# Performance work log

Measured on AMD Instinct MI355X. Metric: run time of the kernel, lower is better.

## Reference

```python
import jax, jax.numpy as jnp
import numpy as np
import itertools

N_SUBSETS = 4
TAU = 0.1


def setup_inputs() -> dict:
    key = jax.random.key(0)
    k1, k2, k3 = jax.random.split(key, 3)
    # scale projections so exp(sim/tau) stays numerically sane (module assumes small/normalized projections)
    projections = jax.random.normal(k1, (8192, 128), dtype=jnp.float32) * 0.05
    xrecon = jax.random.normal(k2, (8192, 784), dtype=jnp.float32)
    recon_label = jax.random.normal(k3, (8192, 784), dtype=jnp.float32)
    return {"projections": projections, "xrecon": xrecon, "recon_label": recon_label}


def _joint_loss(projections, xrecon, recon_label):
    # reconstruction MSE
    recon_loss = jnp.mean(jnp.square(xrecon - recon_label))

    # ---- XNegloss (SimCLR-style with n_subsets positives per group) ----
    N, D = projections.shape
    sim = (projections @ projections.T) / TAU  # [N, N] dot similarity
    gid = jnp.arange(N) // N_SUBSETS
    pos_mask = gid[:, None] == gid[None, :]  # same-group entries are positives
    exp_sim = jnp.exp(sim)
    # original code drops positive entries exactly equal to 1 (positives[positives != 1])
    pos_sum = jnp.sum(jnp.where(pos_mask & (sim != 1.0), exp_sim, 0.0), axis=-1)
    neg_sum = jnp.sum(jnp.where(pos_mask, 0.0, exp_sim), axis=-1)
    closs = jnp.mean(-jnp.log(pos_sum / (pos_sum + neg_sum)))

    # ---- distance loss: MSE over all subset pairs within each group ----
    combi = np.array(list(itertools.combinations(range(N_SUBSETS), 2)))
    left, right = combi[:, 0], combi[:, 1]
    P = projections.reshape(N // N_SUBSETS, N_SUBSETS, D)
    # per-group mean over (pairs, D) then mean over groups == global mean (equal counts)
    dist_loss = jnp.mean(jnp.square(P[:, left] - P[:, right]))

    loss = recon_loss + closs + dist_loss
    return loss, closs, recon_loss, dist_loss


def reference(projections, xrecon, recon_label):
    return _joint_loss(projections, xrecon, recon_label)
```

## Files before the change

kernel.cpp:

```cpp
#include <hip/hip_runtime.h>
#include <hip/hip_bf16.h>
#include <stdint.h>

typedef __bf16 bf16x8 __attribute__((ext_vector_type(8)));
typedef float  f32x4  __attribute__((ext_vector_type(4)));

#define NROWS   8192
#define DIMK    128
#define NGROUPS 2048
#define RECON_N 6422528
#define SIM_BLOCKS   1024
#define RECON_BLOCKS 1568
#define GROUP_BLOCKS 512
#define FUSED_BLOCKS 3104

#define WS_SP     0
#define WS_G      131072
#define WS_E      139264
#define WS_RPART  147456
#define WS_DPART  149024
#define WS_PB     149536

__device__ __forceinline__ void async16(const void* g, void* l) {
    __builtin_amdgcn_global_load_lds(
        (const __attribute__((address_space(1))) void*)g,
        (__attribute__((address_space(3))) void*)l, 16, 0, 0);
}

__device__ __forceinline__ unsigned short f2bf(float f) {
    union { __hip_bfloat16 h; unsigned short u; } v;
    v.h = __float2bfloat16(f);
    return v.u;
}

__global__ __launch_bounds__(256) void prep_kernel(const float4* __restrict__ Pf,
                                                   uint2* __restrict__ Pb) {
    int idx = blockIdx.x * 256 + threadIdx.x;
    float4 a = Pf[idx];
    uint2 r;
    r.x = (uint32_t)f2bf(a.x) | ((uint32_t)f2bf(a.y) << 16);
    r.y = (uint32_t)f2bf(a.z) | ((uint32_t)f2bf(a.w) << 16);
    Pb[idx] = r;
}

__global__ __launch_bounds__(256, 3) void fused_kernel(
        const unsigned short* __restrict__ Pb,
        const float* __restrict__ Pf,
        const float4* __restrict__ X,
        const float4* __restrict__ Y,
        float* __restrict__ ws) {
    __shared__ unsigned short tile[128 * 128];
    const int bx = blockIdx.x;
    const int wave = threadIdx.x >> 6, lane = threadIdx.x & 63;

    int role, idx;
    if (bx < 3072) {
        int r6 = bx % 6, c6 = bx / 6;
        if (r6 == 0)      { role = 0; idx = c6 * 2; }
        else if (r6 == 3) { role = 0; idx = c6 * 2 + 1; }
        else if (r6 == 5) { role = 2; idx = c6; }
        else              { role = 1; idx = c6 * 3 + (r6 == 1 ? 0 : (r6 == 2 ? 1 : 2)); }
    } else {
        role = 1; idx = 1536 + (bx - 3072);
    }

    if (role == 0) {
        __shared__ float sred[2][2][64];
        float* Sp = ws + WS_SP;
        const int wr = wave >> 1, wc = wave & 1;
        const int rowBase = (idx >> 4) * 128;
        const int colBase = (idx & 15) * 512;
        const int m = lane & 15, kq = lane >> 4;

        bf16x8 Af[4][4];
#pragma unroll
        for (int i = 0; i < 4; ++i) {
            const unsigned short* rowp =
                Pb + (size_t)(rowBase + wr * 64 + i * 16 + m) * DIMK + kq * 8;
#pragma unroll
            for (int kk = 0; kk < 4; ++kk)
                Af[i][kk] = *(const bf16x8*)(rowp + kk * 32);
        }

        int srcOff[8];
#pragma unroll
        for (int i = 0; i < 8; ++i) {
            int chunk = (i * 4 + wave) * 64 + lane;
            int r = chunk >> 4, qp = chunk & 15;
            srcOff[i] = r * 256 + (((qp - r) & 15) << 4);
        }

        float rowAcc[4][4];
#pragma unroll
        for (int i = 0; i < 4; ++i)
#pragma unroll
            for (int r = 0; r < 4; ++r) rowAcc[i][r] = 0.f;

        for (int t = 0; t < 4; ++t) {
            {
                const char* g = (const char*)(Pb + (size_t)(colBase + t * 128) * DIMK);
#pragma unroll
                for (int i = 0; i < 8; ++i) {
                    int seg = i * 4 + wave;
                    async16(g + srcOff[i], (char*)tile + seg * 1024 + lane * 16);
                }
            }
            __syncthreads();

#pragma unroll
            for (int j = 0; j < 4; ++j) {
                int rl = wc * 64 + j * 16 + m;
                bf16x8 Bf[4];
#pragma unroll
                for (int kk = 0; kk < 4; ++kk)
                    Bf[kk] = *(const bf16x8*)((const char*)tile + rl * 256 +
                                              (((kq + kk * 4 + rl) & 15) << 4));
                f32x4 acc[4];
#pragma unroll
                for (int i = 0; i < 4; ++i) acc[i] = (f32x4){0.f, 0.f, 0.f, 0.f};
#pragma unroll
                for (int kk = 0; kk < 4; ++kk)
#pragma unroll
                    for (int i = 0; i < 4; ++i)
                        acc[i] = __builtin_amdgcn_mfma_f32_16x16x32_bf16(
                            Af[i][kk], Bf[kk], acc[i], 0, 0, 0);
#pragma unroll
                for (int i = 0; i < 4; ++i)
#pragma unroll
                    for (int r = 0; r < 4; ++r)
                        rowAcc[i][r] += __expf(acc[i][r] * 10.0f);
            }
            __syncthreads();
        }

#pragma unroll
        for (int i = 0; i < 4; ++i)
#pragma unroll
            for (int r = 0; r < 4; ++r) {
                float sv = rowAcc[i][r];
                sv += __shfl_xor(sv, 1, 64);
                sv += __shfl_xor(sv, 2, 64);
                sv += __shfl_xor(sv, 4, 64);
                sv += __shfl_xor(sv, 8, 64);
                rowAcc[i][r] = sv;
            }
        if ((lane & 15) == 0) {
            int c = lane >> 4;
#pragma unroll
            for (int i = 0; i < 4; ++i)
#pragma unroll
                for (int r = 0; r < 4; ++r)
                    sred[wc][wr][i * 16 + c * 4 + r] = rowAcc[i][r];
        }
        __syncthreads();
        if (wc == 0) {
            float v = sred[0][wr][lane] + sred[1][wr][lane];
            Sp[(size_t)(idx & 15) * NROWS + rowBase + wr * 64 + lane] = v;
        }
    } else if (role == 1) {
        __shared__ float red[4];
        int base = idx * 1024 + threadIdx.x;
        float4 a0 = X[base],       b0 = Y[base];
        float4 a1 = X[base + 256], b1 = Y[base + 256];
        float4 a2 = X[base + 512], b2 = Y[base + 512];
        float4 a3 = X[base + 768], b3 = Y[base + 768];
        float s = 0.f, d;
        d = a0.x - b0.x; s += d * d;  d = a0.y - b0.y; s += d * d;
        d = a0.z - b0.z; s += d * d;  d = a0.w - b0.w; s += d * d;
        d = a1.x - b1.x; s += d * d;  d = a1.y - b1.y; s += d * d;
        d = a1.z - b1.z; s += d * d;  d = a1.w - b1.w; s += d * d;
        d = a2.x - b2.x; s += d * d;  d = a2.y - b2.y; s += d * d;
        d = a2.z - b2.z; s += d * d;  d = a2.w - b2.w; s += d * d;
        d = a3.x - b3.x; s += d * d;  d = a3.y - b3.y; s += d * d;
        d = a3.z - b3.z; s += d * d;  d = a3.w - b3.w; s += d * d;
#pragma unroll
        for (int mm = 1; mm < 64; mm <<= 1) s += __shfl_xor(s, mm, 64);
        if (lane == 0) red[wave] = s;
        __syncthreads();
        if (threadIdx.x == 0)
            ws[WS_RPART + idx] = red[0] + red[1] + red[2] + red[3];
    } else {
        __shared__ float dred[4];
        float* G = ws + WS_G;
        float* E = ws + WS_E;
        int g = idx * 4 + wave;
        const float* base = Pf + (size_t)g * 4 * DIMK;
        float v[4][2];
#pragma unroll
        for (int r = 0; r < 4; ++r) {
            v[r][0] = base[r * DIMK + lane];
            v[r][1] = base[r * DIMK + 64 + lane];
        }
        float dmat[4][4];
#pragma unroll
        for (int r = 0; r < 4; ++r)
#pragma unroll
            for (int s2 = r; s2 < 4; ++s2) {
                float p = v[r][0] * v[s2][0] + v[r][1] * v[s2][1];
#pragma unroll
                for (int mm = 1; mm < 64; mm <<= 1) p += __shfl_xor(p, mm, 64);
                dmat[r][s2] = p; dmat[s2][r] = p;
            }
        if (lane == 0) {
            float distp = 0.f;
#pragma unroll
            for (int r = 0; r < 4; ++r)
#pragma unroll
                for (int s2 = r + 1; s2 < 4; ++s2)
                    distp += dmat[r][r] + dmat[s2][s2] - 2.f * dmat[r][s2];
            dred[wave] = distp;
#pragma unroll
            for (int r = 0; r < 4; ++r) {
                float Gs = 0.f, Es = 0.f;
#pragma unroll
                for (int s2 = 0; s2 < 4; ++s2) {
                    float sim = dmat[r][s2] * 10.0f;
                    float e = __expf(sim);
                    Gs += e;
                    if (sim == 1.0f) Es += e;
                }
                G[g * 4 + r] = Gs;
                E[g * 4 + r] = Es;
            }
        }
        __syncthreads();
        if (threadIdx.x == 0)
            ws[WS_DPART + idx] = dred[0] + dred[1] + dred[2] + dred[3];
    }
}

__global__ __launch_bounds__(1024) void finalize_kernel(const float* __restrict__ ws,
                                                        float* __restrict__ out) {
    __shared__ float redc[16], redr[16], redd[16];
    const float* Sp = ws + WS_SP;
    const float* G  = ws + WS_G;
    const float* E  = ws + WS_E;

    float c = 0.f;
    for (int r = threadIdx.x; r < NROWS; r += 1024) {
        float Sv = 0.f;
#pragma unroll
        for (int q = 0; q < 16; ++q) Sv += Sp[q * NROWS + r];
        c += __logf(Sv - E[r]) - __logf(G[r] - E[r]);
    }
    float rs = 0.f;
    for (int i = threadIdx.x; i < RECON_BLOCKS; i += 1024) rs += ws[WS_RPART + i];
    float ds = 0.f;
    for (int i = threadIdx.x; i < GROUP_BLOCKS; i += 1024) ds += ws[WS_DPART + i];

#pragma unroll
    for (int mm = 1; mm < 64; mm <<= 1) {
        c  += __shfl_xor(c,  mm, 64);
        rs += __shfl_xor(rs, mm, 64);
        ds += __shfl_xor(ds, mm, 64);
    }
    int wave = threadIdx.x >> 6, lane = threadIdx.x & 63;
    if (lane == 0) { redc[wave] = c; redr[wave] = rs; redd[wave] = ds; }
    __syncthreads();
    if (threadIdx.x == 0) {
        float cs = 0.f, rss = 0.f, dss = 0.f;
#pragma unroll
        for (int i = 0; i < 16; ++i) { cs += redc[i]; rss += redr[i]; dss += redd[i]; }
        float closs = cs / (float)NROWS;
        float recon = rss / (float)RECON_N;
        float dist  = dss / (float)(NGROUPS * 6 * DIMK);
        out[0] = recon + closs + dist;
        out[1] = closs;
        out[2] = recon;
        out[3] = dist;
    }
}

extern "C" void kernel_launch(void* const* d_in, const int* in_sizes, int n_in,
                              void* d_out, int out_size, void* d_ws, size_t ws_size,
                              hipStream_t stream) {
    const float* P  = (const float*)d_in[0];
    const float4* X = (const float4*)d_in[1];
    const float4* Y = (const float4*)d_in[2];
    float* out = (float*)d_out;
    float* w = (float*)d_ws;
    unsigned short* Pb = (unsigned short*)(w + WS_PB);

    prep_kernel<<<1024, 256, 0, stream>>>((const float4*)P, (uint2*)Pb);
    fused_kernel<<<FUSED_BLOCKS, 256, 0, stream>>>(Pb, P, X, Y, w);
    finalize_kernel<<<1, 1024, 0, stream>>>(w, out);
}
```

Baseline: 127.1 us.

## Exploit Gram matrix symmetry: compute upper-triangle tiles with row/column atomic sums

Because the similarity matrix is symmetric, the kernel now computes only the 2080 upper-triangular 128x128 tiles instead of the full matrix. Each tile's exp values are reduced along both rows and columns and added into a per-row sum buffer with atomics, so the 16-way partial-sum array and its reduction in finalize are dropped. The row-sum buffer is zeroed in the prep kernel, and exp is computed with a direct exp2 intrinsic. This roughly halves the MFMA and exp work, at the cost of atomics, a triangular index decode and extra column-reduction shuffles.

```diff
diff --git a/kernel.cpp b/kernel.cpp
--- a/kernel.cpp
+++ b/kernel.cpp
@@ -7,19 +7,18 @@
 
 #define NROWS   8192
 #define DIMK    128
-#define NGROUPS 2048
 #define RECON_N 6422528
-#define SIM_BLOCKS   1024
 #define RECON_BLOCKS 1568
 #define GROUP_BLOCKS 512
-#define FUSED_BLOCKS 3104
-
-#define WS_SP     0
-#define WS_G      131072
-#define WS_E      139264
-#define WS_RPART  147456
-#define WS_DPART  149024
-#define WS_PB     149536
+#define SIM_TILES    2080
+#define FUSED_BLOCKS 4160
+
+#define WS_RS     0
+#define WS_G      8192
+#define WS_E      16384
+#define WS_RPART  24576
+#define WS_DPART  26144
+#define WS_PB     26656
 
 __device__ __forceinline__ void async16(const void* g, void* l) {
     __builtin_amdgcn_global_load_lds(
@@ -34,8 +33,10 @@
 }
 
 __global__ __launch_bounds__(256) void prep_kernel(const float4* __restrict__ Pf,
-                                                   uint2* __restrict__ Pb) {
+                                                   uint2* __restrict__ Pb,
+                                                   float* __restrict__ ws) {
     int idx = blockIdx.x * 256 + threadIdx.x;
+    if (blockIdx.x < 32) ws[WS_RS + idx] = 0.f;
     float4 a = Pf[idx];
     uint2 r;
     r.x = (uint32_t)f2bf(a.x) | ((uint32_t)f2bf(a.y) << 16);
@@ -50,87 +51,93 @@
         const float4* __restrict__ Y,
         float* __restrict__ ws) {
     __shared__ unsigned short tile[128 * 128];
+    __shared__ float sred[2][2][64];
+    __shared__ float cred[2][128];
     const int bx = blockIdx.x;
     const int wave = threadIdx.x >> 6, lane = threadIdx.x & 63;
 
     int role, idx;
-    if (bx < 3072) {
-        int r6 = bx % 6, c6 = bx / 6;
-        if (r6 == 0)      { role = 0; idx = c6 * 2; }
-        else if (r6 == 3) { role = 0; idx = c6 * 2 + 1; }
-        else if (r6 == 5) { role = 2; idx = c6; }
-        else              { role = 1; idx = c6 * 3 + (r6 == 1 ? 0 : (r6 == 2 ? 1 : 2)); }
+    if (bx < 4096) {
+        int r8 = bx & 7, c8 = bx >> 3;
+        if ((r8 & 1) == 0)      { role = 0; idx = c8 * 4 + (r8 >> 1); }
+        else if (r8 == 7)       { role = 2; idx = c8; }
+        else                    { role = 1; idx = c8 * 3 + ((r8 - 1) >> 1); }
+    } else if (bx < 4128) {
+        role = 0; idx = 2048 + (bx - 4096);
     } else {
-        role = 1; idx = 1536 + (bx - 3072);
+        role = 1; idx = 1536 + (bx - 4128);
     }
 
     if (role == 0) {
-        __shared__ float sred[2][2][64];
-        float* Sp = ws + WS_SP;
+        float* RS = ws + WS_RS;
+        float ff = 64.5f - sqrtf(64.5f * 64.5f - 2.0f * (float)idx);
+        int I = (int)ff;
+        int base = I * 64 - (I * (I - 1)) / 2;
+        if (idx < base) { --I; base = I * 64 - (I * (I - 1)) / 2; }
+        else { int nb = (I + 1) * 64 - ((I + 1) * I) / 2;
+               if (idx >= nb) { ++I; base = nb; } }
+        const int J = I + (idx - base);
+
         const int wr = wave >> 1, wc = wave & 1;
-        const int rowBase = (idx >> 4) * 128;
-        const int colBase = (idx & 15) * 512;
         const int m = lane & 15, kq = lane >> 4;
 
+        const char* gB = (const char*)(Pb + (size_t)J * 128 * DIMK);
+#pragma unroll
+        for (int i = 0; i < 8; ++i) {
+            int chunk = i * 256 + wave * 64 + lane;
+            int r = chunk >> 4, qp = chunk & 15;
+            async16(gB + r * 256 + (((qp - r) & 15) << 4),
+                    (char*)tile + chunk * 16);
+        }
+
         bf16x8 Af[4][4];
+        const unsigned short* gA = Pb + (size_t)(I * 128 + wr * 64) * DIMK;
 #pragma unroll
         for (int i = 0; i < 4; ++i) {
-            const unsigned short* rowp =
-                Pb + (size_t)(rowBase + wr * 64 + i * 16 + m) * DIMK + kq * 8;
+            const unsigned short* rowp = gA + (size_t)(i * 16 + m) * DIMK + kq * 8;
 #pragma unroll
             for (int kk = 0; kk < 4; ++kk)
                 Af[i][kk] = *(const bf16x8*)(rowp + kk * 32);
         }
 
-        int srcOff[8];
-#pragma unroll
-        for (int i = 0; i < 8; ++i) {
-            int chunk = (i * 4 + wave) * 64 + lane;
-            int r = chunk >> 4, qp = chunk & 15;
-            srcOff[i] = r * 256 + (((qp - r) & 15) << 4);
-        }
-
         float rowAcc[4][4];
+        float colAcc[4];
 #pragma unroll
         for (int i = 0; i < 4; ++i)
 #pragma unroll
             for (int r = 0; r < 4; ++r) rowAcc[i][r] = 0.f;
 
-        for (int t = 0; t < 4; ++t) {
-            {
-                const char* g = (const char*)(Pb + (size_t)(colBase + t * 128) * DIMK);
-#pragma unroll
-                for (int i = 0; i < 8; ++i) {
-                    int seg = i * 4 + wave;
-                    async16(g + srcOff[i], (char*)tile + seg * 1024 + lane * 16);
+        __syncthreads();
+
+#pragma unroll
+        for (int j = 0; j < 4; ++j) {
+            int rl = wc * 64 + j * 16 + m;
+            bf16x8 Bf[4];
+#pragma unroll
+            for (int kk = 0; kk < 4; ++kk)
+                Bf[kk] = *(const bf16x8*)((const char*)tile + rl * 256 +
+                                          (((kq + kk * 4 + rl) & 15) << 4));
+            f32x4 acc[4];
+#pragma unroll
+            for (int i = 0; i < 4; ++i) acc[i] = (f32x4){0.f, 0.f, 0.f, 0.f};
+#pragma unroll
+            for (int kk = 0; kk < 4; ++kk)
+#pragma unroll
+                for (int i = 0; i < 4; ++i)
+                    acc[i] = __builtin_amdgcn_mfma_f32_16x16x32_bf16(
+                        Af[i][kk], Bf[kk], acc[i], 0, 0, 0);
+            float cs = 0.f;
+#pragma unroll
+            for (int i = 0; i < 4; ++i)
+#pragma unroll
+                for (int r = 0; r < 4; ++r) {
+                    float e = __builtin_amdgcn_exp2f(acc[i][r] * 14.426950408889634f);
+                    rowAcc[i][r] += e;
+                    cs += e;
                 }
-            }
-            __syncthreads();
-
-#pragma unroll
-            for (int j = 0; j < 4; ++j) {
-                int rl = wc * 64 + j * 16 + m;
-                bf16x8 Bf[4];
-#pragma unroll
-                for (int kk = 0; kk < 4; ++kk)
-                    Bf[kk] = *(const bf16x8*)((const char*)tile + rl * 256 +
-                                              (((kq + kk * 4 + rl) & 15) << 4));
-                f32x4 acc[4];
-#pragma unroll
-                for (int i = 0; i < 4; ++i) acc[i] = (f32x4){0.f, 0.f, 0.f, 0.f};
-#pragma unroll
-                for (int kk = 0; kk < 4; ++kk)
-#pragma unroll
-                    for (int i = 0; i < 4; ++i)
-                        acc[i] = __builtin_amdgcn_mfma_f32_16x16x32_bf16(
-                            Af[i][kk], Bf[kk], acc[i], 0, 0, 0);
-#pragma unroll
-                for (int i = 0; i < 4; ++i)
-#pragma unroll
-                    for (int r = 0; r < 4; ++r)
-                        rowAcc[i][r] += __expf(acc[i][r] * 10.0f);
-            }
-            __syncthreads();
+            cs += __shfl_xor(cs, 16, 64);
+            cs += __shfl_xor(cs, 32, 64);
+            colAcc[j] = cs;
         }
 
 #pragma unroll
@@ -144,18 +151,26 @@
                 sv += __shfl_xor(sv, 8, 64);
                 rowAcc[i][r] = sv;
             }
-        if ((lane & 15) == 0) {
-            int c = lane >> 4;
+        if (m == 0) {
 #pragma unroll
             for (int i = 0; i < 4; ++i)
 #pragma unroll
                 for (int r = 0; r < 4; ++r)
-                    sred[wc][wr][i * 16 + c * 4 + r] = rowAcc[i][r];
+                    sred[wc][wr][i * 16 + kq * 4 + r] = rowAcc[i][r];
+        }
+        if (kq == 0) {
+#pragma unroll
+            for (int j = 0; j < 4; ++j)
+                cred[wr][wc * 64 + j * 16 + m] = colAcc[j];
         }
         __syncthreads();
         if (wc == 0) {
             float v = sred[0][wr][lane] + sred[1][wr][lane];
-            Sp[(size_t)(idx & 15) * NROWS + rowBase + wr * 64 + lane] = v;
+            atomicAdd(&RS[I * 128 + wr * 64 + lane], v);
+        } else if (I != J) {
+            int col = wr * 64 + lane;
+            float v = cred[0][col] + cred[1][col];
+            atomicAdd(&RS[J * 128 + col], v);
         }
     } else if (role == 1) {
         __shared__ float red[4];
@@ -232,15 +247,13 @@
 __global__ __launch_bounds__(1024) void finalize_kernel(const float* __restrict__ ws,
                                                         float* __restrict__ out) {
     __shared__ float redc[16], redr[16], redd[16];
-    const float* Sp = ws + WS_SP;
+    const float* RS = ws + WS_RS;
     const float* G  = ws + WS_G;
     const float* E  = ws + WS_E;
 
     float c = 0.f;
     for (int r = threadIdx.x; r < NROWS; r += 1024) {
-        float Sv = 0.f;
-#pragma unroll
-        for (int q = 0; q < 16; ++q) Sv += Sp[q * NROWS + r];
+        float Sv = RS[r];
         c += __logf(Sv - E[r]) - __logf(G[r] - E[r]);
     }
     float rs = 0.f;
@@ -263,7 +276,7 @@
         for (int i = 0; i < 16; ++i) { cs += redc[i]; rss += redr[i]; dss += redd[i]; }
         float closs = cs / (float)NROWS;
         float recon = rss / (float)RECON_N;
-        float dist  = dss / (float)(NGROUPS * 6 * DIMK);
+        float dist  = dss / (float)(2048 * 6 * DIMK);
         out[0] = recon + closs + dist;
         out[1] = closs;
         out[2] = recon;
@@ -281,7 +294,7 @@
     float* w = (float*)d_ws;
     unsigned short* Pb = (unsigned short*)(w + WS_PB);
 
-    prep_kernel<<<1024, 256, 0, stream>>>((const float4*)P, (uint2*)Pb);
+    prep_kernel<<<1024, 256, 0, stream>>>((const float4*)P, (uint2*)Pb, w);
     fused_kernel<<<FUSED_BLOCKS, 256, 0, stream>>>(Pb, P, X, Y, w);
     finalize_kernel<<<1, 1024, 0, stream>>>(w, out);
 }
```

Result: no change. 129.0 us (+1.5%).
